# Kernel tuning notes

Hardware: AMD Instinct MI355X
Metric: run time of the kernel (lower is better)

The kernel has to match this reference:

```python
import math
import jax, jax.numpy as jnp
import numpy as np

D_MODEL = 1024
N_HEAD = 16
HEAD_DIM = D_MODEL // N_HEAD
MAX_LENGTH = 2048


def sinusoid_table():
    # Matches RelativeEmbedding.get_embedding with num_embeddings = max_length + 1
    num_emb = MAX_LENGTH + 1
    half = HEAD_DIM // 2
    freq = jnp.exp(jnp.arange(half, dtype=jnp.float32) * (-math.log(10000.0) / (half - 1)))
    lo = -((num_emb + 1) // 2)  # python floor of -num_emb//2
    hi = num_emb // 2
    pos = jnp.arange(lo, hi, dtype=jnp.float32)  # length num_emb
    ang = pos[:, None] * freq[None, :]
    table = jnp.concatenate([jnp.sin(ang), jnp.cos(ang)], axis=1)  # (num_emb, HEAD_DIM)
    origin_shift = num_emb // 2 + 1
    return table, origin_shift


def _shift(BD):
    # (b, n, L, 2L) -> (b, n, L, L) diagonal-shift trick
    b, n, L, _ = BD.shape
    BD = jnp.concatenate([BD, jnp.zeros((b, n, L, 1), BD.dtype)], axis=-1)
    BD = BD.reshape(b, n, -1, L)[:, :, :-1, :].reshape(b, n, L, -1)
    return BD[:, :, :, :L]


def setup_inputs() -> dict:
    key = jax.random.key(0)
    k1, k2, k3, k4 = jax.random.split(key, 4)
    B, L = 2, 1024
    x = jax.random.normal(k1, (B, L, D_MODEL), dtype=jnp.float32)
    mask = jnp.ones((B, L), dtype=jnp.int32)
    W_qv = jax.random.normal(k2, (2 * D_MODEL, D_MODEL), dtype=jnp.float32) * 0.02
    r_r_bias = jax.random.normal(k3, (N_HEAD, HEAD_DIM), dtype=jnp.float32) * 0.02
    r_w_bias = jax.random.normal(k4, (N_HEAD, HEAD_DIM), dtype=jnp.float32) * 0.02
    return {"x": x, "mask": mask, "W_qv": W_qv, "r_r_bias": r_r_bias, "r_w_bias": r_w_bias}


def reference(x, mask, W_qv, r_r_bias, r_w_bias):
    B, L, d = x.shape
    table, origin_shift = sinusoid_table()
    pos = jnp.arange(-L, L) + origin_shift
    pos_embed = table[pos]  # (2L, head_dim)

    qv = x @ W_qv.T  # (B, L, 2d)
    q, v = jnp.split(qv, 2, axis=-1)
    q = q.reshape(B, L, N_HEAD, HEAD_DIM).transpose(0, 2, 1, 3)  # (B,H,L,dh)
    k = x.reshape(B, L, N_HEAD, HEAD_DIM).transpose(0, 2, 1, 3)
    v = v.reshape(B, L, N_HEAD, HEAD_DIM).transpose(0, 2, 1, 3)

    AC = jnp.einsum('bnqd,bnkd->bnqk', q + r_r_bias[None, :, None, :], k)
    D_ = jnp.einsum('nd,ld->nl', r_w_bias, pos_embed)[None, :, None, :]  # (1,H,1,2L)
    B_ = jnp.einsum('bnqd,ld->bnql', q, pos_embed)  # (B,H,L,2L)
    BD = _shift(B_ + D_)

    attn = AC + BD
    attn = jnp.where(mask[:, None, None, :] == 0, -jnp.inf, attn)
    attn = jax.nn.softmax(attn, axis=-1)
    out = jnp.einsum('bnqk,bnkd->bnqd', attn, v)
    return out.transpose(0, 2, 1, 3).reshape(B, L, d)
```

## Files before the change

### kernel.cpp

```cpp
#include <hip/hip_runtime.h>
#include <hip/hip_bf16.h>
#include <math.h>

#define L_SEQ 1024
#define TWO_L 2048
#define NHEAD 16
#define HD 64
#define DM 1024
#define BATCH 2
#define PE2R 2176

typedef _Float16 f16;
typedef _Float16 f16x4 __attribute__((ext_vector_type(4)));
typedef _Float16 f16x8 __attribute__((ext_vector_type(8)));
typedef float f32x4 __attribute__((ext_vector_type(4)));

__device__ __forceinline__ f16x8 ld8(const f16* p) {
  f16x4 lo = *(const f16x4*)p;
  f16x4 hi = *(const f16x4*)(p + 16);
  f16x8 r;
  r[0] = lo[0]; r[1] = lo[1]; r[2] = lo[2]; r[3] = lo[3];
  r[4] = hi[0]; r[5] = hi[1]; r[6] = hi[2]; r[7] = hi[3];
  return r;
}

__device__ __forceinline__ float pe_val(int j, int d) {
  float posval = (float)(j - L_SEQ);
  float freq = expf(-(float)(d & 31) * 0.2971077539347156f);
  float ang = posval * freq;
  return (d < 32) ? sinf(ang) : cosf(ang);
}

__global__ __launch_bounds__(256) void prep1(const float* __restrict__ x,
                                             const float* __restrict__ W,
                                             f16* __restrict__ pe2,
                                             f16* __restrict__ xh,
                                             f16* __restrict__ Wh) {
  int bid = blockIdx.x, tid = threadIdx.x;
  if (bid < 2048) {
    int i = (bid * 256 + tid) * 4;
    float4 v = *(const float4*)(x + i);
    f16x4 o = {(f16)v.x, (f16)v.y, (f16)v.z, (f16)v.w};
    *(f16x4*)(xh + i) = o;
  } else if (bid < 4096) {
    int i = ((bid - 2048) * 256 + tid) * 4;
    float4 v = *(const float4*)(W + i);
    f16x4 o = {(f16)v.x, (f16)v.y, (f16)v.z, (f16)v.w};
    *(f16x4*)(Wh + i) = o;
  } else {
    int idx = (bid - 4096) * 256 + tid;
    int rrow = idx >> 6, d = idx & 63;
    int u = rrow - 1088;
    int j = (u < 0) ? u + 2049 : u;
    float v = (j != 2048) ? pe_val(j, d) : 0.f;
    pe2[idx] = (f16)v;
  }
}

#define QV_STEP(T, AS, BS, CA0, CA1, CB0, CB1, NA0, NA1, NB0, NB1)             \
  {                                                                            \
    *(f16x8*)&AS[r * 72 + c] = CA0;                                            \
    *(f16x8*)&AS[r * 72 + c + 8] = CA1;                                        \
    *(f16x8*)&BS[r * 72 + c] = CB0;                                            \
    *(f16x8*)&BS[r * 72 + c + 8] = CB1;                                        \
    __syncthreads();                                                           \
    if ((T) + 1 < 16) {                                                        \
      const f16* na = ga + ((T) + 1) * 64;                                     \
      NA0 = *(const f16x8*)na;                                                 \
      NA1 = *(const f16x8*)(na + 8);                                           \
      const f16* nb = gb + ((T) + 1) * 64;                                     \
      NB0 = *(const f16x8*)nb;                                                 \
      NB1 = *(const f16x8*)(nb + 8);                                           \
    }                                                                          \
    _Pragma("unroll")                                                          \
    for (int kc = 0; kc < 2; ++kc) {                                           \
      f16x8 a = ld8(&AS[(w * 16 + li) * 72 + kc * 32 + g * 4]);                \
      _Pragma("unroll")                                                        \
      for (int nf = 0; nf < 4; ++nf) {                                         \
        f16x8 bfr = ld8(&BS[(nf * 16 + li) * 72 + kc * 32 + g * 4]);           \
        s[nf] = __builtin_amdgcn_mfma_f32_16x16x32_f16(a, bfr, s[nf], 0, 0, 0);\
      }                                                                        \
    }                                                                          \
  }

__global__ __launch_bounds__(256) void qv_mfma(const f16* __restrict__ xh,
                                               const f16* __restrict__ Wh,
                                               f16* __restrict__ qvh,
                                               f16* __restrict__ vT) {
  __shared__ f16 As0[64 * 72], As1[64 * 72];
  __shared__ f16 Bs0[64 * 72], Bs1[64 * 72];
  int tid = threadIdx.x;
  int w = tid >> 6, lane = tid & 63, g = lane >> 4, li = lane & 15;
  int m0 = blockIdx.y * 64, n0 = blockIdx.x * 64;
  int r = tid >> 2, c = (tid & 3) * 16;

  const f16* ga = xh + (size_t)(m0 + r) * 1024 + c;
  const f16* gb = Wh + (size_t)(n0 + r) * 1024 + c;
  f16x8 ca0 = *(const f16x8*)ga, ca1 = *(const f16x8*)(ga + 8);
  f16x8 cb0 = *(const f16x8*)gb, cb1 = *(const f16x8*)(gb + 8);
  f16x8 na0, na1, nb0, nb1;

  f32x4 s[4];
#pragma unroll
  for (int i = 0; i < 4; ++i) s[i] = {0.f, 0.f, 0.f, 0.f};

  for (int t = 0; t < 16; t += 2) {
    QV_STEP(t, As0, Bs0, ca0, ca1, cb0, cb1, na0, na1, nb0, nb1);
    QV_STEP(t + 1, As1, Bs1, na0, na1, nb0, nb1, ca0, ca1, cb0, cb1);
  }

#pragma unroll
  for (int nf = 0; nf < 4; ++nf) {
    int n = n0 + nf * 16 + li;
#pragma unroll
    for (int rr2 = 0; rr2 < 4; ++rr2) {
      int m = m0 + w * 16 + g * 4 + rr2;
      f16 val = (f16)s[nf][rr2];
      if (n < 1024) {
        qvh[(size_t)m * 2048 + n] = val;
      } else {
        int b_ = m >> 10, ls = m & 1023, hd = n - 1024;
        vT[((size_t)(b_ * 16 + (hd >> 6)) * 64 + (hd & 63)) * 1024 + ls] = val;
      }
    }
  }
}

#define BANDFILL(TT, QOFF, PEREG)                                              \
  {                                                                            \
    _Pragma("unroll")                                                          \
    for (int qf = 0; qf < 4; ++qf) {                                           \
      f32x4 gacc = {0.f, 0.f, 0.f, 0.f};                                       \
      _Pragma("unroll")                                                        \
      for (int kc = 0; kc < 2; ++kc) {                                         \
        f16x8 qo = ld8(&Qw[((QOFF) + qf * 16 + li) * 72 + kc * 32 + g * 4]);   \
        gacc = __builtin_amdgcn_mfma_f32_16x16x32_f16(PEREG[kc], qo, gacc, 0, 0, 0); \
      }                                                                        \
      f16x4 gpk;                                                               \
      gpk[0] = (f16)gacc[0]; gpk[1] = (f16)gacc[1];                            \
      gpk[2] = (f16)gacc[2]; gpk[3] = (f16)gacc[3];                            \
      *(f16x4*)&Gb[(qf * 16 + li) * 136 + (TT) + w * 16 + g * 4] = gpk;        \
    }                                                                          \
  }

#define ATTN_STEP(T, KS, VS, CK0, CK1, CV0, CV1, NK0, NK1, NV0, NV1, CPE, NPE) \
  {                                                                            \
    const int k0 = (T) * 64;                                                   \
    const int tt = (64 * (T)) & 127;                                           \
    const int qoff = (64 * (T) >= q0) ? 1 : 0;                                 \
    *(f16x8*)&KS[r * 72 + c] = CK0;                                            \
    *(f16x8*)&KS[r * 72 + c + 8] = CK1;                                        \
    *(f16x8*)&VS[r * 72 + c] = CV0;                                            \
    *(f16x8*)&VS[r * 72 + c + 8] = CV1;                                        \
    BANDFILL(tt, qoff, CPE)                                                    \
    __syncthreads();                                                           \
    if ((T) + 1 < 16) {                                                        \
      const f16* nk = gk + (size_t)((T) + 1) * 64 * 1024;                      \
      NK0 = *(const f16x8*)nk;                                                 \
      NK1 = *(const f16x8*)(nk + 8);                                           \
      const f16* nv = gv + ((T) + 1) * 64;                                     \
      NV0 = *(const f16x8*)nv;                                                 \
      NV1 = *(const f16x8*)(nv + 8);                                           \
      const f16* pb = pe2 + (size_t)(1088 + 64 * ((T) + 1) - q0 + w * 16 + li) * 64; \
      NPE[0] = ld8(pb + g * 4);                                                \
      NPE[1] = ld8(pb + 32 + g * 4);                                           \
    }                                                                          \
    float gf[16];                                                              \
    {                                                                          \
      const int cb0 = tt + g * 4 - qi + 128;                                   \
      _Pragma("unroll")                                                        \
      for (int kf = 0; kf < 4; ++kf)                                           \
        _Pragma("unroll")                                                      \
        for (int u2 = 0; u2 < 4; ++u2)                                         \
          gf[kf * 4 + u2] = (float)Gb[qi * 136 + ((cb0 + kf * 16 + u2) & 127)];\
    }                                                                          \
    f32x4 s[4];                                                                \
    _Pragma("unroll")                                                          \
    for (int i = 0; i < 4; ++i) s[i] = {0.f, 0.f, 0.f, 0.f};                   \
    __builtin_amdgcn_s_setprio(1);                                             \
    _Pragma("unroll")                                                          \
    for (int kc = 0; kc < 2; ++kc) {                                           \
      f16x8 qb = ld8(&Qs[(1 + w * 16 + li) * 72 + kc * 32 + g * 4]);           \
      _Pragma("unroll")                                                        \
      for (int kf = 0; kf < 4; ++kf) {                                         \
        f16x8 ka = ld8(&KS[(kf * 16 + li) * 72 + kc * 32 + g * 4]);            \
        s[kf] = __builtin_amdgcn_mfma_f32_16x16x32_f16(ka, qb, s[kf], 0, 0, 0);\
      }                                                                        \
    }                                                                          \
    __builtin_amdgcn_s_setprio(0);                                             \
    float sv[16];                                                              \
    float tmax = -1e30f;                                                       \
    _Pragma("unroll")                                                          \
    for (int kf = 0; kf < 4; ++kf) {                                           \
      _Pragma("unroll")                                                        \
      for (int rr2 = 0; rr2 < 4; ++rr2) {                                      \
        float v_ = s[kf][rr2] + gf[kf * 4 + rr2] +                             \
                   Ms[k0 + kf * 16 + g * 4 + rr2];                             \
        sv[kf * 4 + rr2] = v_;                                                 \
        tmax = fmaxf(tmax, v_);                                                \
      }                                                                        \
    }                                                                          \
    tmax = fmaxf(tmax, __shfl_xor(tmax, 16));                                  \
    tmax = fmaxf(tmax, __shfl_xor(tmax, 32));                                  \
    float mnew = fmaxf(m_run, tmax);                                           \
    float scale = __expf(m_run - mnew);                                        \
    m_run = mnew;                                                              \
    l_run *= scale;                                                            \
    _Pragma("unroll")                                                          \
    for (int f = 0; f < 4; ++f) {                                              \
      o[f][0] *= scale; o[f][1] *= scale; o[f][2] *= scale; o[f][3] *= scale;  \
    }                                                                          \
    float pf[16];                                                              \
    float lloc = 0.f;                                                          \
    _Pragma("unroll")                                                          \
    for (int i = 0; i < 16; ++i) { pf[i] = __expf(sv[i] - mnew); lloc += pf[i]; } \
    l_run += lloc;                                                             \
    f16x8 pb0, pb1;                                                            \
    _Pragma("unroll")                                                          \
    for (int i = 0; i < 8; ++i) { pb0[i] = (f16)pf[i]; pb1[i] = (f16)pf[8 + i]; } \
    __builtin_amdgcn_s_setprio(1);                                             \
    _Pragma("unroll")                                                          \
    for (int f = 0; f < 4; ++f) {                                              \
      f16x8 va0 = ld8(&VS[(f * 16 + li) * 72 + g * 4]);                        \
      o[f] = __builtin_amdgcn_mfma_f32_16x16x32_f16(va0, pb0, o[f], 0, 0, 0);  \
      f16x8 va1 = ld8(&VS[(f * 16 + li) * 72 + 32 + g * 4]);                   \
      o[f] = __builtin_amdgcn_mfma_f32_16x16x32_f16(va1, pb1, o[f], 0, 0, 0);  \
    }                                                                          \
    __builtin_amdgcn_s_setprio(0);                                             \
    __syncthreads();                                                           \
  }

__global__ __launch_bounds__(256) void attn_mfma(const f16* __restrict__ xh,
                                                 const f16* __restrict__ qvh,
                                                 const f16* __restrict__ vT,
                                                 const f16* __restrict__ pe2,
                                                 const int* __restrict__ mask,
                                                 const float* __restrict__ rr,
                                                 const float* __restrict__ rw,
                                                 float* __restrict__ out) {
  __shared__ f16 Qs[65 * 72];
  __shared__ f16 Qw[65 * 72];
  __shared__ f16 Ks0[64 * 72], Ks1[64 * 72];
  __shared__ f16 Vs0[64 * 72], Vs1[64 * 72];
  __shared__ f16 Gb[64 * 136];
  __shared__ float Ms[L_SEQ];
  int tid = threadIdx.x;
  int w = tid >> 6, lane = tid & 63, g = lane >> 4, li = lane & 15;
  int bh = blockIdx.y, b = bh >> 4, h = bh & 15;
  int q0 = blockIdx.x * 64;
  int r = tid >> 2, c = (tid & 3) * 16;
  const int qi = w * 16 + li;

#pragma unroll
  for (int i = 0; i < 4; ++i) {
    int k = tid + i * 256;
    Ms[k] = mask[b * L_SEQ + k] ? 0.f : -1e30f;
  }
  {
    int gq = q0 - 1 + r;
    if (gq < 0) gq = 0;
    const f16* src = qvh + (size_t)(b * L_SEQ + gq) * 2048 + h * HD + c;
#pragma unroll
    for (int u = 0; u < 16; ++u) {
      float v = (float)src[u];
      Qs[r * 72 + c + u] = (f16)(v + rr[h * HD + c + u]);
      Qw[r * 72 + c + u] = (f16)(v + rw[h * HD + c + u]);
    }
    if (tid < 4) {
      int c2 = tid * 16;
      const f16* s2 = qvh + (size_t)(b * L_SEQ + q0 + 63) * 2048 + h * HD + c2;
#pragma unroll
      for (int u = 0; u < 16; ++u) {
        float v = (float)s2[u];
        Qs[64 * 72 + c2 + u] = (f16)(v + rr[h * HD + c2 + u]);
        Qw[64 * 72 + c2 + u] = (f16)(v + rw[h * HD + c2 + u]);
      }
    }
  }

  const f16* gk = xh + (size_t)(b * L_SEQ + r) * 1024 + h * HD + c;
  const f16* gv = vT + ((size_t)bh * 64 + r) * 1024 + c;
  f16x8 cka = *(const f16x8*)gk, ckb = *(const f16x8*)(gk + 8);
  f16x8 cva = *(const f16x8*)gv, cvb = *(const f16x8*)(gv + 8);
  f16x8 nka, nkb, nva, nvb;
  f16x8 peP[2], peA[2], peB[2];
  {
    const f16* pp = pe2 + (size_t)(1024 - q0 + w * 16 + li) * 64;
    peP[0] = ld8(pp + g * 4);
    peP[1] = ld8(pp + 32 + g * 4);
    const f16* p0 = pe2 + (size_t)(1088 - q0 + w * 16 + li) * 64;
    peA[0] = ld8(p0 + g * 4);
    peA[1] = ld8(p0 + 32 + g * 4);
  }

  __syncthreads();

  BANDFILL(64, 0, peP)

  float m_run = -1e30f, l_run = 0.f;
  f32x4 o[4];
#pragma unroll
  for (int i = 0; i < 4; ++i) o[i] = {0.f, 0.f, 0.f, 0.f};

  for (int t = 0; t < 16; t += 2) {
    ATTN_STEP(t, Ks0, Vs0, cka, ckb, cva, cvb, nka, nkb, nva, nvb, peA, peB);
    ATTN_STEP(t + 1, Ks1, Vs1, nka, nkb, nva, nvb, cka, ckb, cva, cvb, peB, peA);
  }

  float lt = l_run;
  lt += __shfl_xor(lt, 16);
  lt += __shfl_xor(lt, 32);
  float inv = 1.0f / lt;
  int qrow = q0 + qi;
  float* op = out + ((size_t)(b * L_SEQ + qrow)) * DM + h * HD;
#pragma unroll
  for (int f = 0; f < 4; ++f) {
    float4 res = {o[f][0] * inv, o[f][1] * inv, o[f][2] * inv, o[f][3] * inv};
    *(float4*)(op + f * 16 + g * 4) = res;
  }
}

extern "C" void kernel_launch(void* const* d_in, const int* in_sizes, int n_in,
                              void* d_out, int out_size, void* d_ws, size_t ws_size,
                              hipStream_t stream) {
  const float* x = (const float*)d_in[0];
  const int* mask = (const int*)d_in[1];
  const float* W = (const float*)d_in[2];
  const float* rr = (const float*)d_in[3];
  const float* rw = (const float*)d_in[4];
  float* out = (float*)d_out;

  f16* pe2 = (f16*)d_ws;
  f16* xh = pe2 + (size_t)PE2R * 64;
  f16* Wh = xh + 2097152;
  f16* qvh = Wh + 2097152;
  f16* vT = qvh + 4194304;

  prep1<<<4096 + (PE2R * 64) / 256, 256, 0, stream>>>(x, W, pe2, xh, Wh);
  qv_mfma<<<dim3(32, 32), 256, 0, stream>>>(xh, Wh, qvh, vT);
  attn_mfma<<<dim3(16, 32), 256, 0, stream>>>(xh, qvh, vT, pe2, mask, rr, rw, out);
}
```

Baseline: 85.58 us.

## Restructure attention kernel with per-wave band buffers, single buffering and lazy rescale

```diff
diff --git a/kernel.cpp b/kernel.cpp
--- a/kernel.cpp
+++ b/kernel.cpp
@@ -126,129 +126,27 @@
   }
 }
 
-#define BANDFILL(TT, QOFF, PEREG)                                              \
-  {                                                                            \
-    _Pragma("unroll")                                                          \
-    for (int qf = 0; qf < 4; ++qf) {                                           \
-      f32x4 gacc = {0.f, 0.f, 0.f, 0.f};                                       \
-      _Pragma("unroll")                                                        \
-      for (int kc = 0; kc < 2; ++kc) {                                         \
-        f16x8 qo = ld8(&Qw[((QOFF) + qf * 16 + li) * 72 + kc * 32 + g * 4]);   \
-        gacc = __builtin_amdgcn_mfma_f32_16x16x32_f16(PEREG[kc], qo, gacc, 0, 0, 0); \
-      }                                                                        \
-      f16x4 gpk;                                                               \
-      gpk[0] = (f16)gacc[0]; gpk[1] = (f16)gacc[1];                            \
-      gpk[2] = (f16)gacc[2]; gpk[3] = (f16)gacc[3];                            \
-      *(f16x4*)&Gb[(qf * 16 + li) * 136 + (TT) + w * 16 + g * 4] = gpk;        \
-    }                                                                          \
-  }
-
-#define ATTN_STEP(T, KS, VS, CK0, CK1, CV0, CV1, NK0, NK1, NV0, NV1, CPE, NPE) \
-  {                                                                            \
-    const int k0 = (T) * 64;                                                   \
-    const int tt = (64 * (T)) & 127;                                           \
-    const int qoff = (64 * (T) >= q0) ? 1 : 0;                                 \
-    *(f16x8*)&KS[r * 72 + c] = CK0;                                            \
-    *(f16x8*)&KS[r * 72 + c + 8] = CK1;                                        \
-    *(f16x8*)&VS[r * 72 + c] = CV0;                                            \
-    *(f16x8*)&VS[r * 72 + c + 8] = CV1;                                        \
-    BANDFILL(tt, qoff, CPE)                                                    \
-    __syncthreads();                                                           \
-    if ((T) + 1 < 16) {                                                        \
-      const f16* nk = gk + (size_t)((T) + 1) * 64 * 1024;                      \
-      NK0 = *(const f16x8*)nk;                                                 \
-      NK1 = *(const f16x8*)(nk + 8);                                           \
-      const f16* nv = gv + ((T) + 1) * 64;                                     \
-      NV0 = *(const f16x8*)nv;                                                 \
-      NV1 = *(const f16x8*)(nv + 8);                                           \
-      const f16* pb = pe2 + (size_t)(1088 + 64 * ((T) + 1) - q0 + w * 16 + li) * 64; \
-      NPE[0] = ld8(pb + g * 4);                                                \
-      NPE[1] = ld8(pb + 32 + g * 4);                                           \
-    }                                                                          \
-    float gf[16];                                                              \
-    {                                                                          \
-      const int cb0 = tt + g * 4 - qi + 128;                                   \
-      _Pragma("unroll")                                                        \
-      for (int kf = 0; kf < 4; ++kf)                                           \
-        _Pragma("unroll")                                                      \
-        for (int u2 = 0; u2 < 4; ++u2)                                         \
-          gf[kf * 4 + u2] = (float)Gb[qi * 136 + ((cb0 + kf * 16 + u2) & 127)];\
-    }                                                                          \
-    f32x4 s[4];                                                                \
-    _Pragma("unroll")                                                          \
-    for (int i = 0; i < 4; ++i) s[i] = {0.f, 0.f, 0.f, 0.f};                   \
-    __builtin_amdgcn_s_setprio(1);                                             \
-    _Pragma("unroll")                                                          \
-    for (int kc = 0; kc < 2; ++kc) {                                           \
-      f16x8 qb = ld8(&Qs[(1 + w * 16 + li) * 72 + kc * 32 + g * 4]);           \
-      _Pragma("unroll")                                                        \
-      for (int kf = 0; kf < 4; ++kf) {                                         \
-        f16x8 ka = ld8(&KS[(kf * 16 + li) * 72 + kc * 32 + g * 4]);            \
-        s[kf] = __builtin_amdgcn_mfma_f32_16x16x32_f16(ka, qb, s[kf], 0, 0, 0);\
-      }                                                                        \
-    }                                                                          \
-    __builtin_amdgcn_s_setprio(0);                                             \
-    float sv[16];                                                              \
-    float tmax = -1e30f;                                                       \
-    _Pragma("unroll")                                                          \
-    for (int kf = 0; kf < 4; ++kf) {                                           \
-      _Pragma("unroll")                                                        \
-      for (int rr2 = 0; rr2 < 4; ++rr2) {                                      \
-        float v_ = s[kf][rr2] + gf[kf * 4 + rr2] +                             \
-                   Ms[k0 + kf * 16 + g * 4 + rr2];                             \
-        sv[kf * 4 + rr2] = v_;                                                 \
-        tmax = fmaxf(tmax, v_);                                                \
-      }                                                                        \
-    }                                                                          \
-    tmax = fmaxf(tmax, __shfl_xor(tmax, 16));                                  \
-    tmax = fmaxf(tmax, __shfl_xor(tmax, 32));                                  \
-    float mnew = fmaxf(m_run, tmax);                                           \
-    float scale = __expf(m_run - mnew);                                        \
-    m_run = mnew;                                                              \
-    l_run *= scale;                                                            \
-    _Pragma("unroll")                                                          \
-    for (int f = 0; f < 4; ++f) {                                              \
-      o[f][0] *= scale; o[f][1] *= scale; o[f][2] *= scale; o[f][3] *= scale;  \
-    }                                                                          \
-    float pf[16];                                                              \
-    float lloc = 0.f;                                                          \
-    _Pragma("unroll")                                                          \
-    for (int i = 0; i < 16; ++i) { pf[i] = __expf(sv[i] - mnew); lloc += pf[i]; } \
-    l_run += lloc;                                                             \
-    f16x8 pb0, pb1;                                                            \
-    _Pragma("unroll")                                                          \
-    for (int i = 0; i < 8; ++i) { pb0[i] = (f16)pf[i]; pb1[i] = (f16)pf[8 + i]; } \
-    __builtin_amdgcn_s_setprio(1);                                             \
-    _Pragma("unroll")                                                          \
-    for (int f = 0; f < 4; ++f) {                                              \
-      f16x8 va0 = ld8(&VS[(f * 16 + li) * 72 + g * 4]);                        \
-      o[f] = __builtin_amdgcn_mfma_f32_16x16x32_f16(va0, pb0, o[f], 0, 0, 0);  \
-      f16x8 va1 = ld8(&VS[(f * 16 + li) * 72 + 32 + g * 4]);                   \
-      o[f] = __builtin_amdgcn_mfma_f32_16x16x32_f16(va1, pb1, o[f], 0, 0, 0);  \
-    }                                                                          \
-    __builtin_amdgcn_s_setprio(0);                                             \
-    __syncthreads();                                                           \
-  }
-
-__global__ __launch_bounds__(256) void attn_mfma(const f16* __restrict__ xh,
-                                                 const f16* __restrict__ qvh,
-                                                 const f16* __restrict__ vT,
-                                                 const f16* __restrict__ pe2,
-                                                 const int* __restrict__ mask,
-                                                 const float* __restrict__ rr,
-                                                 const float* __restrict__ rw,
-                                                 float* __restrict__ out) {
-  __shared__ f16 Qs[65 * 72];
-  __shared__ f16 Qw[65 * 72];
-  __shared__ f16 Ks0[64 * 72], Ks1[64 * 72];
-  __shared__ f16 Vs0[64 * 72], Vs1[64 * 72];
-  __shared__ f16 Gb[64 * 136];
+__global__ __launch_bounds__(256, 3) void attn_mfma(const f16* __restrict__ xh,
+                                                    const f16* __restrict__ qvh,
+                                                    const f16* __restrict__ vT,
+                                                    const f16* __restrict__ pe2,
+                                                    const int* __restrict__ mask,
+                                                    const float* __restrict__ rr,
+                                                    const float* __restrict__ rw,
+                                                    float* __restrict__ out) {
+  __shared__ f16 Qs[64 * 72];
+  __shared__ f16 Ks[64 * 72], Vs[64 * 72];
+  __shared__ f16 Gbw[4][16 * 132];
   __shared__ float Ms[L_SEQ];
   int tid = threadIdx.x;
   int w = tid >> 6, lane = tid & 63, g = lane >> 4, li = lane & 15;
-  int bh = blockIdx.y, b = bh >> 4, h = bh & 15;
-  int q0 = blockIdx.x * 64;
+  int bid = blockIdx.x;
+  int swz = (bid & 7) * 64 + (bid >> 3);
+  int q0 = (swz & 15) * 64;
+  int bh = swz >> 4;
+  int b = bh >> 4, h = bh & 15;
   int r = tid >> 2, c = (tid & 3) * 16;
+  const int qs0 = q0 + w * 16;
   const int qi = w * 16 + li;
 
 #pragma unroll
@@ -257,54 +155,150 @@
     Ms[k] = mask[b * L_SEQ + k] ? 0.f : -1e30f;
   }
   {
-    int gq = q0 - 1 + r;
-    if (gq < 0) gq = 0;
-    const f16* src = qvh + (size_t)(b * L_SEQ + gq) * 2048 + h * HD + c;
-#pragma unroll
-    for (int u = 0; u < 16; ++u) {
-      float v = (float)src[u];
-      Qs[r * 72 + c + u] = (f16)(v + rr[h * HD + c + u]);
-      Qw[r * 72 + c + u] = (f16)(v + rw[h * HD + c + u]);
-    }
-    if (tid < 4) {
-      int c2 = tid * 16;
-      const f16* s2 = qvh + (size_t)(b * L_SEQ + q0 + 63) * 2048 + h * HD + c2;
-#pragma unroll
-      for (int u = 0; u < 16; ++u) {
-        float v = (float)s2[u];
-        Qs[64 * 72 + c2 + u] = (f16)(v + rr[h * HD + c2 + u]);
-        Qw[64 * 72 + c2 + u] = (f16)(v + rw[h * HD + c2 + u]);
-      }
-    }
+    const f16* src = qvh + (size_t)(b * L_SEQ + q0 + r) * 2048 + h * HD + c;
+#pragma unroll
+    for (int u = 0; u < 16; ++u)
+      Qs[r * 72 + c + u] = (f16)((float)src[u] + rr[h * HD + c + u]);
+  }
+
+  f16x8 qn[2], qw_[2];
+  {
+    int qm1 = qs0 + li - 1;
+    if (qm1 < 0) qm1 = 0;
+    const f16* rnp = qvh + (size_t)(b * L_SEQ + qs0 + li) * 2048 + h * HD;
+    const f16* rwp2 = qvh + (size_t)(b * L_SEQ + qm1) * 2048 + h * HD;
+#pragma unroll
+    for (int kc = 0; kc < 2; ++kc) {
+      f16x8 an = ld8(rnp + kc * 32 + g * 4);
+      f16x8 aw = ld8(rwp2 + kc * 32 + g * 4);
+#pragma unroll
+      for (int e = 0; e < 8; ++e) {
+        int off = kc * 32 + g * 4 + (e & 3) + 16 * (e >> 2);
+        float rwv = rw[h * HD + off];
+        qn[kc][e] = (f16)((float)an[e] + rwv);
+        qw_[kc][e] = (f16)((float)aw[e] + rwv);
+      }
+    }
+  }
+
+#define LOAD_PE(BASE)                                                          \
+  {                                                                            \
+    _Pragma("unroll")                                                          \
+    for (int uf = 0; uf < 4; ++uf) {                                           \
+      const f16* pp = pe2 + (size_t)(1088 + (BASE) + uf * 16 + li) * 64 + g * 4; \
+      pef[uf * 2 + 0] = ld8(pp);                                               \
+      pef[uf * 2 + 1] = ld8(pp + 32);                                          \
+    }                                                                          \
+  }
+
+#define BANDFILL(BASE)                                                         \
+  {                                                                            \
+    _Pragma("unroll")                                                          \
+    for (int uf = 0; uf < 4; ++uf) {                                           \
+      f32x4 gacc = {0.f, 0.f, 0.f, 0.f};                                       \
+      if ((BASE) + uf * 16 < 0) {                                              \
+        gacc = __builtin_amdgcn_mfma_f32_16x16x32_f16(pef[uf * 2], qw_[0], gacc, 0, 0, 0); \
+        gacc = __builtin_amdgcn_mfma_f32_16x16x32_f16(pef[uf * 2 + 1], qw_[1], gacc, 0, 0, 0); \
+      } else {                                                                 \
+        gacc = __builtin_amdgcn_mfma_f32_16x16x32_f16(pef[uf * 2], qn[0], gacc, 0, 0, 0); \
+        gacc = __builtin_amdgcn_mfma_f32_16x16x32_f16(pef[uf * 2 + 1], qn[1], gacc, 0, 0, 0); \
+      }                                                                        \
+      int cu0 = ((BASE) + uf * 16 + g * 4 + 2048) & 127;                       \
+      f16x4 gpk = {(f16)gacc[0], (f16)gacc[1], (f16)gacc[2], (f16)gacc[3]};    \
+      *(f16x4*)&Gbw[w][li * 132 + cu0] = gpk;                                  \
+    }                                                                          \
   }
 
   const f16* gk = xh + (size_t)(b * L_SEQ + r) * 1024 + h * HD + c;
   const f16* gv = vT + ((size_t)bh * 64 + r) * 1024 + c;
-  f16x8 cka = *(const f16x8*)gk, ckb = *(const f16x8*)(gk + 8);
-  f16x8 cva = *(const f16x8*)gv, cvb = *(const f16x8*)(gv + 8);
-  f16x8 nka, nkb, nva, nvb;
-  f16x8 peP[2], peA[2], peB[2];
-  {
-    const f16* pp = pe2 + (size_t)(1024 - q0 + w * 16 + li) * 64;
-    peP[0] = ld8(pp + g * 4);
-    peP[1] = ld8(pp + 32 + g * 4);
-    const f16* p0 = pe2 + (size_t)(1088 - q0 + w * 16 + li) * 64;
-    peA[0] = ld8(p0 + g * 4);
-    peA[1] = ld8(p0 + 32 + g * 4);
-  }
-
-  __syncthreads();
-
-  BANDFILL(64, 0, peP)
+  f16x8 ck0 = *(const f16x8*)gk, ck1 = *(const f16x8*)(gk + 8);
+  f16x8 cv0 = *(const f16x8*)gv, cv1 = *(const f16x8*)(gv + 8);
+
+  f16x8 pef[8];
+  LOAD_PE(-qs0 - 64)
+  BANDFILL(-qs0 - 64)
+  LOAD_PE(-qs0)
 
   float m_run = -1e30f, l_run = 0.f;
   f32x4 o[4];
 #pragma unroll
   for (int i = 0; i < 4; ++i) o[i] = {0.f, 0.f, 0.f, 0.f};
 
-  for (int t = 0; t < 16; t += 2) {
-    ATTN_STEP(t, Ks0, Vs0, cka, ckb, cva, cvb, nka, nkb, nva, nvb, peA, peB);
-    ATTN_STEP(t + 1, Ks1, Vs1, nka, nkb, nva, nvb, cka, ckb, cva, cvb, peB, peA);
+  for (int t = 0; t < 16; ++t) {
+    const int k0 = t * 64;
+    const int base = k0 - qs0;
+    __syncthreads();
+    *(f16x8*)&Ks[r * 72 + c] = ck0;
+    *(f16x8*)&Ks[r * 72 + c + 8] = ck1;
+    *(f16x8*)&Vs[r * 72 + c] = cv0;
+    *(f16x8*)&Vs[r * 72 + c + 8] = cv1;
+    BANDFILL(base)
+    __syncthreads();
+    if (t < 15) {
+      const f16* nk = gk + (size_t)(t + 1) * 64 * 1024;
+      ck0 = *(const f16x8*)nk;
+      ck1 = *(const f16x8*)(nk + 8);
+      const f16* nv = gv + (t + 1) * 64;
+      cv0 = *(const f16x8*)nv;
+      cv1 = *(const f16x8*)(nv + 8);
+      LOAD_PE(base + 64)
+    }
+    f32x4 s[4];
+#pragma unroll
+    for (int i = 0; i < 4; ++i) s[i] = {0.f, 0.f, 0.f, 0.f};
+    __builtin_amdgcn_s_setprio(1);
+#pragma unroll
+    for (int kc = 0; kc < 2; ++kc) {
+      f16x8 qb = ld8(&Qs[(w * 16 + li) * 72 + kc * 32 + g * 4]);
+#pragma unroll
+      for (int kf = 0; kf < 4; ++kf) {
+        f16x8 ka = ld8(&Ks[(kf * 16 + li) * 72 + kc * 32 + g * 4]);
+        s[kf] = __builtin_amdgcn_mfma_f32_16x16x32_f16(ka, qb, s[kf], 0, 0, 0);
+      }
+    }
+    __builtin_amdgcn_s_setprio(0);
+    const int gbase = base + g * 4 - li + 2048;
+    float sv[16];
+    float tmax = -1e30f;
+#pragma unroll
+    for (int kf = 0; kf < 4; ++kf) {
+#pragma unroll
+      for (int u2 = 0; u2 < 4; ++u2) {
+        float gfv = (float)Gbw[w][li * 132 + ((gbase + kf * 16 + u2) & 127)];
+        float v_ = s[kf][u2] + gfv + Ms[k0 + kf * 16 + g * 4 + u2];
+        sv[kf * 4 + u2] = v_;
+        tmax = fmaxf(tmax, v_);
+      }
+    }
+    tmax = fmaxf(tmax, __shfl_xor(tmax, 16));
+    tmax = fmaxf(tmax, __shfl_xor(tmax, 32));
+    if (!__all(tmax <= m_run + 8.f)) {
+      float mnew = fmaxf(m_run, tmax);
+      float scale = __expf(m_run - mnew);
+      m_run = mnew;
+      l_run *= scale;
+#pragma unroll
+      for (int f = 0; f < 4; ++f) {
+        o[f][0] *= scale; o[f][1] *= scale; o[f][2] *= scale; o[f][3] *= scale;
+      }
+    }
+    float pf[16];
+    float lloc = 0.f;
+#pragma unroll
+    for (int i = 0; i < 16; ++i) { pf[i] = __expf(sv[i] - m_run); lloc += pf[i]; }
+    l_run += lloc;
+    f16x8 pb0, pb1;
+#pragma unroll
+    for (int i = 0; i < 8; ++i) { pb0[i] = (f16)pf[i]; pb1[i] = (f16)pf[8 + i]; }
+    __builtin_amdgcn_s_setprio(1);
+#pragma unroll
+    for (int f = 0; f < 4; ++f) {
+      f16x8 va0 = ld8(&Vs[(f * 16 + li) * 72 + g * 4]);
+      o[f] = __builtin_amdgcn_mfma_f32_16x16x32_f16(va0, pb0, o[f], 0, 0, 0);
+      f16x8 va1 = ld8(&Vs[(f * 16 + li) * 72 + 32 + g * 4]);
+      o[f] = __builtin_amdgcn_mfma_f32_16x16x32_f16(va1, pb1, o[f], 0, 0, 0);
+    }
+    __builtin_amdgcn_s_setprio(0);
   }
 
   float lt = l_run;
@@ -318,6 +312,8 @@
     float4 res = {o[f][0] * inv, o[f][1] * inv, o[f][2] * inv, o[f][3] * inv};
     *(float4*)(op + f * 16 + g * 4) = res;
   }
+#undef LOAD_PE
+#undef BANDFILL
 }
 
 extern "C" void kernel_launch(void* const* d_in, const int* in_sizes, int n_in,
@@ -338,5 +334,5 @@
 
   prep1<<<4096 + (PE2R * 64) / 256, 256, 0, stream>>>(x, W, pe2, xh, Wh);
   qv_mfma<<<dim3(32, 32), 256, 0, stream>>>(xh, Wh, qvh, vT);
-  attn_mfma<<<dim3(16, 32), 256, 0, stream>>>(xh, qvh, vT, pe2, mask, rr, rw, out);
-}
+  attn_mfma<<<512, 256, 0, stream>>>(xh, qvh, vT, pe2, mask, rr, rw, out);
+}
```

New measurement: 114.9 us. 34.2% more time.
